# Kernel tuning notes

Hardware: AMD Instinct MI355X
Metric: run time of the kernel (lower is better)

## Reference

```python
import jax, jax.numpy as jnp
import numpy as np

H, D, C, GROUPS = 8, 80, 640, 32
EPS = 1e-5


def group_norm(x, gamma, beta):
    b, h, w, c = x.shape
    xr = x.reshape(b, h, w, GROUPS, c // GROUPS)
    mean = xr.mean(axis=(1, 2, 4), keepdims=True)
    var = xr.var(axis=(1, 2, 4), keepdims=True)
    xn = ((xr - mean) * jax.lax.rsqrt(var + EPS)).reshape(b, h, w, c)
    return xn * gamma + beta


def layer_norm(x, gamma, beta):
    mean = x.mean(axis=-1, keepdims=True)
    var = x.var(axis=-1, keepdims=True)
    return (x - mean) * jax.lax.rsqrt(var + EPS) * gamma + beta


def cross_attention(x, ctx, wq, wk, wv, wo, bo):
    b, sq, _ = x.shape
    sk = ctx.shape[1]
    q = (x @ wq).reshape(b, sq, H, D)
    k = (ctx @ wk).reshape(b, sk, H, D)
    v = (ctx @ wv).reshape(b, sk, H, D)
    score = jnp.einsum('bqhd,bkhd->bhqk', q, k) * (D ** -0.5)
    w = jax.nn.softmax(score, axis=-1)
    attn = jnp.einsum('bhqk,bkhd->bqhd', w, v).reshape(b, sq, H * D)
    return attn @ wo + bo


def geglu(x, w, bias):
    y = x @ w + bias
    xx, gate = y[..., :4 * C], y[..., 4 * C:]
    tanh_res = jnp.tanh(gate * 0.7978845608 * (1.0 + 0.044715 * gate * gate))
    return xx * 0.5 * gate * (1.0 + tanh_res)


def setup_inputs() -> dict:
    key = jax.random.key(0)
    ks = jax.random.split(key, 32)
    s = 0.02
    inp = {
        'inputs': jax.random.normal(ks[0], (8, 32, 32, C), jnp.float32),
        'context': jax.random.normal(ks[1], (8, 77, 768), jnp.float32),
        'gn_gamma': jnp.ones((C,), jnp.float32),
        'gn_beta': jnp.zeros((C,), jnp.float32),
        'w_proj1': jax.random.normal(ks[2], (C, C), jnp.float32) * s,
        'b_proj1': jnp.zeros((C,), jnp.float32),
        'ln1_g': jnp.ones((C,), jnp.float32), 'ln1_b': jnp.zeros((C,), jnp.float32),
        'wq1': jax.random.normal(ks[3], (C, C), jnp.float32) * s,
        'wk1': jax.random.normal(ks[4], (C, C), jnp.float32) * s,
        'wv1': jax.random.normal(ks[5], (C, C), jnp.float32) * s,
        'wo1': jax.random.normal(ks[6], (C, C), jnp.float32) * s,
        'bo1': jnp.zeros((C,), jnp.float32),
        'ln2_g': jnp.ones((C,), jnp.float32), 'ln2_b': jnp.zeros((C,), jnp.float32),
        'wq2': jax.random.normal(ks[7], (C, C), jnp.float32) * s,
        'wk2': jax.random.normal(ks[8], (768, C), jnp.float32) * s,
        'wv2': jax.random.normal(ks[9], (768, C), jnp.float32) * s,
        'wo2': jax.random.normal(ks[10], (C, C), jnp.float32) * s,
        'bo2': jnp.zeros((C,), jnp.float32),
        'ln3_g': jnp.ones((C,), jnp.float32), 'ln3_b': jnp.zeros((C,), jnp.float32),
        'w_geglu': jax.random.normal(ks[11], (C, 8 * C), jnp.float32) * s,
        'b_geglu': jnp.zeros((8 * C,), jnp.float32),
        'w_ffout': jax.random.normal(ks[12], (4 * C, C), jnp.float32) * s,
        'b_ffout': jnp.zeros((C,), jnp.float32),
        'w_proj2': jax.random.normal(ks[13], (C, C), jnp.float32) * s,
        'b_proj2': jnp.zeros((C,), jnp.float32),
    }
    return inp


def reference(inputs, context, gn_gamma, gn_beta, w_proj1, b_proj1,
              ln1_g, ln1_b, wq1, wk1, wv1, wo1, bo1,
              ln2_g, ln2_b, wq2, wk2, wv2, wo2, bo2,
              ln3_g, ln3_b, w_geglu, b_geglu, w_ffout, b_ffout,
              w_proj2, b_proj2):
    b, h, w, c = inputs.shape
    x = group_norm(inputs, gn_gamma, gn_beta)
    x = x @ w_proj1 + b_proj1  # 1x1 conv == per-pixel dense
    x = x.reshape(b, h * w, c)
    # BasicTransformerBlock
    x = cross_attention(layer_norm(x, ln1_g, ln1_b), layer_norm(x, ln1_g, ln1_b), wq1, wk1, wv1, wo1, bo1) + x
    x = cross_attention(layer_norm(x, ln2_g, ln2_b), context, wq2, wk2, wv2, wo2, bo2) + x
    x = geglu(layer_norm(x, ln3_g, ln3_b), w_geglu, b_geglu) @ w_ffout + b_ffout + x
    x = x.reshape(b, h, w, c)
    return x @ w_proj2 + b_proj2 + inputs
```

## Files before the change

### kernel.cpp

```cpp
#include <hip/hip_runtime.h>
#include <hip/hip_bf16.h>


#define HD 8
#define DHD 80
#define CCH 640
#define SQ 1024

using short8  = __attribute__((ext_vector_type(8))) short;
using floatx4 = __attribute__((ext_vector_type(4))) float;

__device__ __forceinline__ float bf2f(ushort u) {
  union { unsigned int i; float f; } v; v.i = ((unsigned int)u) << 16; return v.f;
}
__device__ __forceinline__ ushort f2bf(float f) {
  union { float f; unsigned int i; } v; v.f = f;
  unsigned int r = v.i + 0x7FFFu + ((v.i >> 16) & 1u);
  return (ushort)(r >> 16);
}
__device__ __forceinline__ float gelu_gate(float g) {
  float z = 0.7978845608f * g * (1.0f + 0.044715f * g * g);
  return g / (1.0f + __expf(-2.0f * z));
}

typedef const __attribute__((address_space(1))) void* gas_ptr;
typedef __attribute__((address_space(3))) void* las_ptr;
__device__ __forceinline__ void gload_lds16(const void* g, void* l) {
  __builtin_amdgcn_global_load_lds((gas_ptr)g, (las_ptr)l, 16, 0, 0);
}

template<int BN>
__global__ __launch_bounds__(256) void gemm_bf16_kernel(
    const ushort* __restrict__ A, const ushort* __restrict__ BT,
    const float* __restrict__ bias, const float* __restrict__ res,
    float* __restrict__ outF, ushort* __restrict__ outB,
    int M, int N, int K, int nby, int q8, int r8)
{
  constexpr int NT  = BN / 32;
  constexpr int LPT = (BN == 128) ? 4 : 3;
  __shared__ ushort As[3][128][32];
  __shared__ ushort Bs[3][BN][32];
  const int tid  = threadIdx.x;
  const int lane = tid & 63;
  const int wave = tid >> 6;
  const int wm = (wave >> 1) * 64, wn = (wave & 1) * (BN / 2);

  const int orig = blockIdx.x;
  const int xcd = orig & 7, bix = orig >> 3;
  const int logical = (xcd < r8) ? xcd * (q8 + 1) + bix
                                 : r8 * (q8 + 1) + (xcd - r8) * q8 + bix;
  const int bm = (logical / nby) * 128;
  const int bn = (logical % nby) * BN;

  const int fr = lane & 15, fk = (lane >> 4) * 8;
  const bool full = (bm + 128 <= M);
  const int nt = K >> 5;

  floatx4 acc[4][NT];
  #pragma unroll
  for (int i = 0; i < 4; ++i)
    #pragma unroll
    for (int j = 0; j < NT; ++j) acc[i][j] = (floatx4){0.f, 0.f, 0.f, 0.f};

  const int lr = lane >> 2, lc = (lane & 3) * 8;
  const ushort* pA0 = A  + (size_t)(bm + wave * 16 + lr) * K + lc;
  const ushort* pA1 = pA0 + (size_t)64 * K;
  const ushort* pB0 = BT + (size_t)(bn + wave * 16 + lr) * K + lc;
  const ushort* pB1 = pB0 + (size_t)64 * K;
  const int r0 = tid >> 2, c0 = (tid & 3) * 8;

  if (full) {
    auto stageF = [&](int nb, int t) {
      const int kt = t * 32;
      gload_lds16(pA0 + kt, &As[nb][wave * 16][0]);
      gload_lds16(pA1 + kt, &As[nb][wave * 16 + 64][0]);
      gload_lds16(pB0 + kt, &Bs[nb][wave * 16][0]);
      if (BN == 128) gload_lds16(pB1 + kt, &Bs[nb][wave * 16 + 64][0]);
    };
    stageF(0, 0);
    if (nt > 1) stageF(1, 1);
    int cb = 0;
    for (int t = 0; t < nt; ++t) {
      if (t + 1 < nt) {
        asm volatile("s_waitcnt vmcnt(%0)" :: "i"(LPT) : "memory");
      } else {
        asm volatile("s_waitcnt vmcnt(0)" ::: "memory");
      }
      __builtin_amdgcn_s_barrier();
      if (t + 2 < nt) stageF((cb + 2 > 2) ? cb - 1 : cb + 2, t + 2);
      short8 af[4], bfr[NT];
      #pragma unroll
      for (int mi = 0; mi < 4; ++mi) af[mi]  = *(const short8*)(&As[cb][wm + mi * 16 + fr][fk]);
      #pragma unroll
      for (int ni = 0; ni < NT; ++ni) bfr[ni] = *(const short8*)(&Bs[cb][wn + ni * 16 + fr][fk]);
      #pragma unroll
      for (int mi = 0; mi < 4; ++mi)
        #pragma unroll
        for (int ni = 0; ni < NT; ++ni)
          acc[mi][ni] = __builtin_amdgcn_mfma_f32_16x16x32_bf16(af[mi], bfr[ni], acc[mi][ni], 0, 0, 0);
      cb = (cb == 2) ? 0 : cb + 1;
    }
  } else {
    auto stageT = [&](int nb, int t) {
      const int kt = t * 32;
      #pragma unroll
      for (int it = 0; it < 2; ++it) {
        int r = r0 + it * 64;
        int gm = bm + r;
        uint4 va = make_uint4(0u, 0u, 0u, 0u);
        if (gm < M) va = *(const uint4*)(A + (size_t)gm * K + kt + c0);
        *(uint4*)(&As[nb][r][c0]) = va;
        if (r < BN) {
          int gn = bn + r;
          uint4 vb = make_uint4(0u, 0u, 0u, 0u);
          if (gn < N) vb = *(const uint4*)(BT + (size_t)gn * K + kt + c0);
          *(uint4*)(&Bs[nb][r][c0]) = vb;
        }
      }
    };
    stageT(0, 0);
    __syncthreads();
    int cur = 0;
    for (int t = 0; t < nt; ++t) {
      if (t + 1 < nt) stageT(cur ^ 1, t + 1);
      short8 af[4], bfr[NT];
      #pragma unroll
      for (int mi = 0; mi < 4; ++mi) af[mi]  = *(const short8*)(&As[cur][wm + mi * 16 + fr][fk]);
      #pragma unroll
      for (int ni = 0; ni < NT; ++ni) bfr[ni] = *(const short8*)(&Bs[cur][wn + ni * 16 + fr][fk]);
      #pragma unroll
      for (int mi = 0; mi < 4; ++mi)
        #pragma unroll
        for (int ni = 0; ni < NT; ++ni)
          acc[mi][ni] = __builtin_amdgcn_mfma_f32_16x16x32_bf16(af[mi], bfr[ni], acc[mi][ni], 0, 0, 0);
      __syncthreads();
      cur ^= 1;
    }
  }

  const int fq = (lane >> 4) * 4;
  #pragma unroll
  for (int mi = 0; mi < 4; ++mi)
    #pragma unroll
    for (int rr = 0; rr < 4; ++rr) {
      int gm = bm + wm + mi * 16 + fq + rr;
      if (gm >= M) continue;
      #pragma unroll
      for (int ni = 0; ni < NT; ++ni) {
        int col = bn + wn + ni * 16 + fr;
        float v = acc[mi][ni][rr];
        if (bias) v += bias[col];
        if (res) v += res[(size_t)gm * N + col];
        size_t o = (size_t)gm * N + col;
        if (outF) outF[o] = v;
        if (outB) outB[o] = f2bf(v);
      }
    }
}

__global__ __launch_bounds__(256) void gemm_geglu_kernel(
    const ushort* __restrict__ A, const ushort* __restrict__ BTx,
    const ushort* __restrict__ BTg, const float* __restrict__ bx,
    const float* __restrict__ bg, ushort* __restrict__ outB,
    int M, int N, int K, int nby, int q8, int r8)
{
  __shared__ ushort As[3][128][32];
  __shared__ ushort Bsx[3][64][32];
  __shared__ ushort Bsg[3][64][32];
  const int tid  = threadIdx.x;
  const int lane = tid & 63;
  const int wave = tid >> 6;
  const int wm = (wave >> 1) * 64, wn = (wave & 1) * 32;

  const int orig = blockIdx.x;
  const int xcd = orig & 7, bix = orig >> 3;
  const int logical = (xcd < r8) ? xcd * (q8 + 1) + bix
                                 : r8 * (q8 + 1) + (xcd - r8) * q8 + bix;
  const int bm = (logical / nby) * 128;
  const int bn = (logical % nby) * 64;

  const int fr = lane & 15, fk = (lane >> 4) * 8;
  const int nt = K >> 5;

  floatx4 accx[4][2], accg[4][2];
  #pragma unroll
  for (int i = 0; i < 4; ++i)
    #pragma unroll
    for (int j = 0; j < 2; ++j) {
      accx[i][j] = (floatx4){0.f, 0.f, 0.f, 0.f};
      accg[i][j] = (floatx4){0.f, 0.f, 0.f, 0.f};
    }

  const int lr = lane >> 2, lc = (lane & 3) * 8;
  const ushort* pA0 = A   + (size_t)(bm + wave * 16 + lr) * K + lc;
  const ushort* pA1 = pA0 + (size_t)64 * K;
  const ushort* pBx = BTx + (size_t)(bn + wave * 16 + lr) * K + lc;
  const ushort* pBg = BTg + (size_t)(bn + wave * 16 + lr) * K + lc;

  auto stageF = [&](int nb, int t) {
    const int kt = t * 32;
    gload_lds16(pA0 + kt, &As[nb][wave * 16][0]);
    gload_lds16(pA1 + kt, &As[nb][wave * 16 + 64][0]);
    gload_lds16(pBx + kt, &Bsx[nb][wave * 16][0]);
    gload_lds16(pBg + kt, &Bsg[nb][wave * 16][0]);
  };
  stageF(0, 0);
  if (nt > 1) stageF(1, 1);
  int cb = 0;
  for (int t = 0; t < nt; ++t) {
    if (t + 1 < nt) {
      asm volatile("s_waitcnt vmcnt(4)" ::: "memory");
    } else {
      asm volatile("s_waitcnt vmcnt(0)" ::: "memory");
    }
    __builtin_amdgcn_s_barrier();
    if (t + 2 < nt) stageF((cb + 2 > 2) ? cb - 1 : cb + 2, t + 2);
    short8 af[4], bfx[2], bfg[2];
    #pragma unroll
    for (int mi = 0; mi < 4; ++mi) af[mi] = *(const short8*)(&As[cb][wm + mi * 16 + fr][fk]);
    #pragma unroll
    for (int ni = 0; ni < 2; ++ni) {
      bfx[ni] = *(const short8*)(&Bsx[cb][wn + ni * 16 + fr][fk]);
      bfg[ni] = *(const short8*)(&Bsg[cb][wn + ni * 16 + fr][fk]);
    }
    #pragma unroll
    for (int mi = 0; mi < 4; ++mi)
      #pragma unroll
      for (int ni = 0; ni < 2; ++ni) {
        accx[mi][ni] = __builtin_amdgcn_mfma_f32_16x16x32_bf16(af[mi], bfx[ni], accx[mi][ni], 0, 0, 0);
        accg[mi][ni] = __builtin_amdgcn_mfma_f32_16x16x32_bf16(af[mi], bfg[ni], accg[mi][ni], 0, 0, 0);
      }
    cb = (cb == 2) ? 0 : cb + 1;
  }

  const int fq = (lane >> 4) * 4;
  #pragma unroll
  for (int mi = 0; mi < 4; ++mi)
    #pragma unroll
    for (int rr = 0; rr < 4; ++rr) {
      int gm = bm + wm + mi * 16 + fq + rr;
      #pragma unroll
      for (int ni = 0; ni < 2; ++ni) {
        int col = bn + wn + ni * 16 + fr;
        float xx = accx[mi][ni][rr] + bx[col];
        float g  = accg[mi][ni][rr] + bg[col];
        outB[(size_t)gm * N + col] = f2bf(xx * gelu_gate(g));
      }
    }
}

#define KVB 64

__global__ __launch_bounds__(256) void attn_mfma_kernel(
    const ushort* __restrict__ Qp, int rsq,
    const ushort* __restrict__ Kp, const ushort* __restrict__ Vp, int rskv,
    ushort* __restrict__ O, int Sq, int Sk)
{
  __shared__ ushort Ks[KVB][104];
  __shared__ ushort Vt[80][88];
  __shared__ ushort Ps[4][16][88];
  const int tid  = threadIdx.x;
  const int lane = tid & 63;
  const int w    = tid >> 6;
  const int l15  = lane & 15;
  const int lg   = lane >> 4;
  const int nqt  = Sq >> 6;
  const int qt   = blockIdx.x % nqt;
  const int bh   = blockIdx.x / nqt;
  const int h    = bh & (HD - 1);
  const int b    = bh / HD;
  const int q0   = qt * 64 + w * 16;

  short8 qf[3];
  #pragma unroll
  for (int kc = 0; kc < 3; ++kc) {
    int d0 = kc * 32 + lg * 8;
    if (d0 < DHD)
      qf[kc] = *(const short8*)(Qp + (size_t)(b * Sq + q0 + l15) * rsq + h * DHD + d0);
    else
      qf[kc] = (short8){0, 0, 0, 0, 0, 0, 0, 0};
  }

  floatx4 oa[5];
  #pragma unroll
  for (int nt = 0; nt < 5; ++nt) oa[nt] = (floatx4){0.f, 0.f, 0.f, 0.f};
  float m[4], lsum[4];
  #pragma unroll
  for (int r = 0; r < 4; ++r) { m[r] = -1e30f; lsum[r] = 0.f; }

  for (int c = tid; c < 128; c += 256)
    *(uint4*)(&Ks[c >> 1][80 + (c & 1) * 8]) = make_uint4(0u, 0u, 0u, 0u);

  for (int kt = 0; kt < Sk; kt += KVB) {
    __syncthreads();
    for (int c = tid; c < 320; c += 256) {
      int row = c / 5, sub = c % 5;
      int kvg = kt + row;
      uint4 v = make_uint4(0u, 0u, 0u, 0u);
      if (kvg < Sk) v = *(const uint4*)(Kp + (size_t)(b * Sk + kvg) * rskv + h * DHD + sub * 8);
      *(uint4*)(&Ks[row][sub * 8]) = v;
    }
    for (int idx = tid; idx < 2560; idx += 256) {
      int d = idx % 80, kv2 = (idx / 80) * 2;
      int kvg = kt + kv2;
      uint pair = 0;
      if (kvg < Sk)     pair  = (uint)Vp[(size_t)(b * Sk + kvg) * rskv + h * DHD + d];
      if (kvg + 1 < Sk) pair |= ((uint)Vp[(size_t)(b * Sk + kvg + 1) * rskv + h * DHD + d]) << 16;
      *(uint*)(&Vt[d][kv2]) = pair;
    }
    __syncthreads();

    short8 kf[4][3];
    #pragma unroll
    for (int nt = 0; nt < 4; ++nt)
      #pragma unroll
      for (int kc = 0; kc < 3; ++kc)
        kf[nt][kc] = *(const short8*)(&Ks[nt * 16 + l15][kc * 32 + lg * 8]);
    floatx4 s[4];
    #pragma unroll
    for (int nt = 0; nt < 4; ++nt) s[nt] = (floatx4){0.f, 0.f, 0.f, 0.f};
    #pragma unroll
    for (int nt = 0; nt < 4; ++nt)
      #pragma unroll
      for (int kc = 0; kc < 3; ++kc)
        s[nt] = __builtin_amdgcn_mfma_f32_16x16x32_bf16(qf[kc], kf[nt][kc], s[nt], 0, 0, 0);

    const bool masked = (kt + KVB > Sk);
    #pragma unroll
    for (int r = 0; r < 4; ++r) {
      float sv[4];
      #pragma unroll
      for (int nt = 0; nt < 4; ++nt) {
        float t = s[nt][r];
        sv[nt] = (masked && (kt + nt * 16 + l15 >= Sk)) ? -1e30f : t;
      }
      float mx = fmaxf(fmaxf(sv[0], sv[1]), fmaxf(sv[2], sv[3]));
      mx = fmaxf(mx, __shfl_xor(mx, 1));
      mx = fmaxf(mx, __shfl_xor(mx, 2));
      mx = fmaxf(mx, __shfl_xor(mx, 4));
      mx = fmaxf(mx, __shfl_xor(mx, 8));
      float mn = fmaxf(m[r], mx);
      float al = __expf(m[r] - mn);
      m[r] = mn;
      float lt = 0.f;
      #pragma unroll
      for (int nt = 0; nt < 4; ++nt) {
        float p = __expf(sv[nt] - mn);
        lt += p;
        Ps[w][lg * 4 + r][nt * 16 + l15] = f2bf(p);
      }
      lt += __shfl_xor(lt, 1);
      lt += __shfl_xor(lt, 2);
      lt += __shfl_xor(lt, 4);
      lt += __shfl_xor(lt, 8);
      lsum[r] = lsum[r] * al + lt;
      #pragma unroll
      for (int nt = 0; nt < 5; ++nt) oa[nt][r] *= al;
    }

    short8 pf[2];
    #pragma unroll
    for (int kc2 = 0; kc2 < 2; ++kc2)
      pf[kc2] = *(const short8*)(&Ps[w][l15][kc2 * 32 + lg * 8]);
    #pragma unroll
    for (int kc2 = 0; kc2 < 2; ++kc2)
      #pragma unroll
      for (int nt = 0; nt < 5; ++nt) {
        short8 vf = *(const short8*)(&Vt[nt * 16 + l15][kc2 * 32 + lg * 8]);
        oa[nt] = __builtin_amdgcn_mfma_f32_16x16x32_bf16(pf[kc2], vf, oa[nt], 0, 0, 0);
      }
  }

  #pragma unroll
  for (int r = 0; r < 4; ++r) {
    float inv = 1.f / lsum[r];
    size_t row = (size_t)(b * Sq + q0 + lg * 4 + r) * CCH + h * DHD;
    #pragma unroll
    for (int nt = 0; nt < 5; ++nt)
      O[row + nt * 16 + l15] = f2bf(oa[nt][r] * inv);
  }
}

__global__ __launch_bounds__(256) void layernorm_kernel(
    const float* __restrict__ X, const float* __restrict__ g,
    const float* __restrict__ bt, ushort* __restrict__ out)
{
  int row  = blockIdx.x * 4 + (threadIdx.x >> 6);
  int lane = threadIdx.x & 63;
  const float* xr = X + (size_t)row * CCH;
  float v[10];
  float s = 0.f, ss = 0.f;
  #pragma unroll
  for (int i = 0; i < 10; ++i) {
    float x = xr[lane + i * 64];
    v[i] = x; s += x; ss += x * x;
  }
  #pragma unroll
  for (int msk = 1; msk < 64; msk <<= 1) { s += __shfl_xor(s, msk); ss += __shfl_xor(ss, msk); }
  float mean = s * (1.f / 640.f);
  float var  = ss * (1.f / 640.f) - mean * mean;
  float rs   = rsqrtf(var + 1e-5f);
  ushort* orow = out + (size_t)row * CCH;
  #pragma unroll
  for (int i = 0; i < 10; ++i) {
    int c = lane + i * 64;
    orow[c] = f2bf((v[i] - mean) * rs * g[c] + bt[c]);
  }
}

__global__ __launch_bounds__(256) void groupnorm_kernel(
    const float* __restrict__ X, const float* __restrict__ gamma,
    const float* __restrict__ beta, ushort* __restrict__ out)
{
  int b = blockIdx.x >> 5;
  int g = blockIdx.x & 31;
  int tid = threadIdx.x;
  const float* base = X + (size_t)b * SQ * CCH + g * 20;
  float s = 0.f, ss = 0.f;
  for (int p = tid; p < SQ; p += 256) {
    const float* rp = base + (size_t)p * CCH;
    #pragma unroll
    for (int c = 0; c < 20; ++c) { float x = rp[c]; s += x; ss += x * x; }
  }
  #pragma unroll
  for (int msk = 1; msk < 64; msk <<= 1) { s += __shfl_xor(s, msk); ss += __shfl_xor(ss, msk); }
  __shared__ float red[2][4];
  int lane = tid & 63, wv = tid >> 6;
  if (lane == 0) { red[0][wv] = s; red[1][wv] = ss; }
  __syncthreads();
  s  = red[0][0] + red[0][1] + red[0][2] + red[0][3];
  ss = red[1][0] + red[1][1] + red[1][2] + red[1][3];
  float mean = s * (1.f / 20480.f);
  float var  = ss * (1.f / 20480.f) - mean * mean;
  float rstd = rsqrtf(var + 1e-5f);
  ushort* ob = out + (size_t)b * SQ * CCH + g * 20;
  for (int p = tid; p < SQ; p += 256) {
    const float* rp = base + (size_t)p * CCH;
    ushort* op = ob + (size_t)p * CCH;
    #pragma unroll
    for (int c = 0; c < 20; ++c)
      op[c] = f2bf((rp[c] - mean) * rstd * gamma[g * 20 + c] + beta[g * 20 + c]);
  }
}

__global__ __launch_bounds__(256) void transpose_cast_kernel(
    const float* __restrict__ W, ushort* __restrict__ WT, int K, int ld,
    int coff, float scale)
{
  __shared__ float tile[32][33];
  const int tx = threadIdx.x, ty = threadIdx.y;
  const int k0 = blockIdx.x * 32, n0 = blockIdx.y * 32;
  #pragma unroll
  for (int i = 0; i < 4; ++i)
    tile[ty + i * 8][tx] = W[(size_t)(k0 + ty + i * 8) * ld + coff + n0 + tx];
  __syncthreads();
  #pragma unroll
  for (int i = 0; i < 4; ++i)
    WT[(size_t)(n0 + ty + i * 8) * K + k0 + tx] = f2bf(tile[tx][ty + i * 8] * scale);
}

__global__ void cast_kernel(const float* __restrict__ X, ushort* __restrict__ Y, int n)
{
  int i = (blockIdx.x * 256 + threadIdx.x) * 4;
  if (i < n) {
    float4 v = *(const float4*)(X + i);
    ushort4 o;
    o.x = f2bf(v.x); o.y = f2bf(v.y); o.z = f2bf(v.z); o.w = f2bf(v.w);
    *(ushort4*)(Y + i) = o;
  }
}

static inline void gemm(hipStream_t st, const ushort* A, const ushort* BT,
                        const float* bias, const float* res,
                        float* outF, ushort* outB, int M, int N, int K)
{
  int nbx = (M + 127) / 128;
  if (N % 128 == 0 && N > 640) {
    int nby = N / 128, nwg = nbx * nby;
    gemm_bf16_kernel<128><<<dim3(nwg), dim3(256), 0, st>>>(
        A, BT, bias, res, outF, outB, M, N, K, nby, nwg / 8, nwg % 8);
  } else {
    int nby = N / 64, nwg = nbx * nby;
    gemm_bf16_kernel<64><<<dim3(nwg), dim3(256), 0, st>>>(
        A, BT, bias, res, outF, outB, M, N, K, nby, nwg / 8, nwg % 8);
  }
}

extern "C" void kernel_launch(void* const* d_in, const int* in_sizes, int n_in,
                              void* d_out, int out_size, void* d_ws, size_t ws_size,
                              hipStream_t stream)
{
  const float* inputs  = (const float*)d_in[0];
  const float* context = (const float*)d_in[1];
  const float* gn_g    = (const float*)d_in[2];
  const float* gn_b    = (const float*)d_in[3];
  const float* w_proj1 = (const float*)d_in[4];
  const float* b_proj1 = (const float*)d_in[5];
  const float* ln1_g   = (const float*)d_in[6];
  const float* ln1_b   = (const float*)d_in[7];
  const float* wq1     = (const float*)d_in[8];
  const float* wk1     = (const float*)d_in[9];
  const float* wv1     = (const float*)d_in[10];
  const float* wo1     = (const float*)d_in[11];
  const float* bo1     = (const float*)d_in[12];
  const float* ln2_g   = (const float*)d_in[13];
  const float* ln2_b   = (const float*)d_in[14];
  const float* wq2     = (const float*)d_in[15];
  const float* wk2     = (const float*)d_in[16];
  const float* wv2     = (const float*)d_in[17];
  const float* wo2     = (const float*)d_in[18];
  const float* bo2     = (const float*)d_in[19];
  const float* ln3_g   = (const float*)d_in[20];
  const float* ln3_b   = (const float*)d_in[21];
  const float* w_geglu = (const float*)d_in[22];
  const float* b_geglu = (const float*)d_in[23];
  const float* w_ffout = (const float*)d_in[24];
  const float* b_ffout = (const float*)d_in[25];
  const float* w_proj2 = (const float*)d_in[26];
  const float* b_proj2 = (const float*)d_in[27];

  const float qscale = 0.11180339887498949f;

  char* p = (char*)d_ws;
  auto alloc = [&](size_t bytes) -> char* {
    char* r = p; p += (bytes + 255) & ~(size_t)255; return r;
  };
  ushort* wT_p1   = (ushort*)alloc(640 * 640 * 2);
  ushort* wT_qkv1 = (ushort*)alloc((size_t)1920 * 640 * 2);
  ushort* wT_o1   = (ushort*)alloc(640 * 640 * 2);
  ushort* wT_q2   = (ushort*)alloc(640 * 640 * 2);
  ushort* wT_kv2  = (ushort*)alloc((size_t)1280 * 768 * 2);
  ushort* wT_o2   = (ushort*)alloc(640 * 640 * 2);
  ushort* wT_gx   = (ushort*)alloc((size_t)2560 * 640 * 2);
  ushort* wT_gg   = (ushort*)alloc((size_t)2560 * 640 * 2);
  ushort* wT_ff   = (ushort*)alloc((size_t)640 * 2560 * 2);
  ushort* wT_p2   = (ushort*)alloc(640 * 640 * 2);
  ushort* ctxb    = (ushort*)alloc((size_t)616 * 768 * 2);
  float*  x       = (float*)alloc((size_t)8192 * 640 * 4);
  ushort* lnb     = (ushort*)alloc((size_t)8192 * 640 * 2);
  ushort* R       = (ushort*)alloc((size_t)8192 * 2560 * 2);
  ushort* kvb     = (ushort*)alloc((size_t)616 * 1280 * 2);
  ushort* qkvb = R;
  ushort* qbx  = R;
  ushort* hb   = R;
  ushort* ab   = lnb;

  auto T = [&](const float* W, ushort* WT, int K, int Nout, int ld, int coff, float sc) {
    dim3 g(K / 32, Nout / 32);
    transpose_cast_kernel<<<g, dim3(32, 8), 0, stream>>>(W, WT, K, ld, coff, sc);
  };
  T(w_proj1, wT_p1, 640, 640, 640, 0, 1.f);
  T(wq1, wT_qkv1,              640, 640, 640, 0, qscale);
  T(wk1, wT_qkv1 + 640 * 640,  640, 640, 640, 0, 1.f);
  T(wv1, wT_qkv1 + 1280 * 640, 640, 640, 640, 0, 1.f);
  T(wo1, wT_o1, 640, 640, 640, 0, 1.f);
  T(wq2, wT_q2, 640, 640, 640, 0, qscale);
  T(wk2, wT_kv2,             768, 640, 640, 0, 1.f);
  T(wv2, wT_kv2 + 640 * 768, 768, 640, 640, 0, 1.f);
  T(wo2, wT_o2, 640, 640, 640, 0, 1.f);
  T(w_geglu, wT_gx, 640, 2560, 5120, 0, 1.f);
  T(w_geglu, wT_gg, 640, 2560, 5120, 2560, 1.f);
  T(w_ffout, wT_ff, 2560, 640, 640, 0, 1.f);
  T(w_proj2, wT_p2, 640, 640, 640, 0, 1.f);
  cast_kernel<<<dim3((616 * 768 / 4 + 255) / 256), dim3(256), 0, stream>>>(context, ctxb, 616 * 768);

  groupnorm_kernel<<<dim3(256), dim3(256), 0, stream>>>(inputs, gn_g, gn_b, lnb);
  gemm(stream, lnb, wT_p1, b_proj1, nullptr, x, nullptr, 8192, 640, 640);

  layernorm_kernel<<<dim3(2048), dim3(256), 0, stream>>>(x, ln1_g, ln1_b, lnb);
  gemm(stream, lnb, wT_qkv1, nullptr, nullptr, nullptr, qkvb, 8192, 1920, 640);
  attn_mfma_kernel<<<dim3(1024), dim3(256), 0, stream>>>(qkvb, 1920, qkvb + 640, qkvb + 1280, 1920, ab, 1024, 1024);
  gemm(stream, ab, wT_o1, bo1, x, x, nullptr, 8192, 640, 640);

  layernorm_kernel<<<dim3(2048), dim3(256), 0, stream>>>(x, ln2_g, ln2_b, lnb);
  gemm(stream, lnb, wT_q2, nullptr, nullptr, nullptr, qbx, 8192, 640, 640);
  gemm(stream, ctxb, wT_kv2, nullptr, nullptr, nullptr, kvb, 616, 1280, 768);
  attn_mfma_kernel<<<dim3(1024), dim3(256), 0, stream>>>(qbx, 640, kvb, kvb + 640, 1280, ab, 1024, 77);
  gemm(stream, ab, wT_o2, bo2, x, x, nullptr, 8192, 640, 640);

  layernorm_kernel<<<dim3(2048), dim3(256), 0, stream>>>(x, ln3_g, ln3_b, lnb);
  {
    int nby = 2560 / 64, nwg = 64 * nby;
    gemm_geglu_kernel<<<dim3(nwg), dim3(256), 0, stream>>>(
        lnb, wT_gx, wT_gg, b_geglu, b_geglu + 2560, hb, 8192, 2560, 640,
        nby, nwg / 8, nwg % 8);
  }
  gemm(stream, hb, wT_ff, b_ffout, x, x, nullptr, 8192, 640, 2560);

  cast_kernel<<<dim3((8192 * 640 / 4 + 255) / 256), dim3(256), 0, stream>>>(x, lnb, 8192 * 640);
  gemm(stream, lnb, wT_p2, b_proj2, inputs, (float*)d_out, nullptr, 8192, 640, 640);
}
```

Baseline: 591.3 us.

## Transpose QK^T MFMA so each lane owns a query row for softmax

Swaps the MFMA operands so the score tile comes out transposed: each lane holds four key scores for a single query row. The online-softmax max and sum then reduce mostly inside the lane, with only two cross-lane shuffles each, instead of four shuffle rounds per row for four rows. Probabilities are packed and written to LDS as uint2 rather than scalar shorts. Rescale factors and the final normalizers are redistributed to the output layout with __shfl. The V-transpose staging loop is also unrolled with incremental index updates to avoid div/mod.

```diff
diff --git a/kernel.cpp b/kernel.cpp
--- a/kernel.cpp
+++ b/kernel.cpp
@@ -284,9 +284,7 @@
   floatx4 oa[5];
   #pragma unroll
   for (int nt = 0; nt < 5; ++nt) oa[nt] = (floatx4){0.f, 0.f, 0.f, 0.f};
-  float m[4], lsum[4];
-  #pragma unroll
-  for (int r = 0; r < 4; ++r) { m[r] = -1e30f; lsum[r] = 0.f; }
+  float m = -1e30f, lsum = 0.f;
 
   for (int c = tid; c < 128; c += 256)
     *(uint4*)(&Ks[c >> 1][80 + (c & 1) * 8]) = make_uint4(0u, 0u, 0u, 0u);
@@ -300,13 +298,19 @@
       if (kvg < Sk) v = *(const uint4*)(Kp + (size_t)(b * Sk + kvg) * rskv + h * DHD + sub * 8);
       *(uint4*)(&Ks[row][sub * 8]) = v;
     }
-    for (int idx = tid; idx < 2560; idx += 256) {
-      int d = idx % 80, kv2 = (idx / 80) * 2;
-      int kvg = kt + kv2;
-      uint pair = 0;
-      if (kvg < Sk)     pair  = (uint)Vp[(size_t)(b * Sk + kvg) * rskv + h * DHD + d];
-      if (kvg + 1 < Sk) pair |= ((uint)Vp[(size_t)(b * Sk + kvg + 1) * rskv + h * DHD + d]) << 16;
-      *(uint*)(&Vt[d][kv2]) = pair;
+    {
+      int d = tid % 80;
+      int kv2 = (tid / 80) * 2;
+      const ushort* vpb = Vp + (size_t)(b * Sk + kt) * rskv + h * DHD;
+      #pragma unroll
+      for (int it = 0; it < 10; ++it) {
+        int kvg = kt + kv2;
+        uint pair = 0;
+        if (kvg < Sk)     pair  = (uint)vpb[(size_t)kv2 * rskv + d];
+        if (kvg + 1 < Sk) pair |= ((uint)vpb[(size_t)(kv2 + 1) * rskv + d]) << 16;
+        *(uint*)(&Vt[d][kv2]) = pair;
+        if (d >= 64) { d -= 64; kv2 += 8; } else { d += 16; kv2 += 6; }
+      }
     }
     __syncthreads();
 
@@ -323,40 +327,50 @@
     for (int nt = 0; nt < 4; ++nt)
       #pragma unroll
       for (int kc = 0; kc < 3; ++kc)
-        s[nt] = __builtin_amdgcn_mfma_f32_16x16x32_bf16(qf[kc], kf[nt][kc], s[nt], 0, 0, 0);
-
-    const bool masked = (kt + KVB > Sk);
-    #pragma unroll
-    for (int r = 0; r < 4; ++r) {
-      float sv[4];
-      #pragma unroll
-      for (int nt = 0; nt < 4; ++nt) {
-        float t = s[nt][r];
-        sv[nt] = (masked && (kt + nt * 16 + l15 >= Sk)) ? -1e30f : t;
-      }
-      float mx = fmaxf(fmaxf(sv[0], sv[1]), fmaxf(sv[2], sv[3]));
-      mx = fmaxf(mx, __shfl_xor(mx, 1));
-      mx = fmaxf(mx, __shfl_xor(mx, 2));
-      mx = fmaxf(mx, __shfl_xor(mx, 4));
-      mx = fmaxf(mx, __shfl_xor(mx, 8));
-      float mn = fmaxf(m[r], mx);
-      float al = __expf(m[r] - mn);
-      m[r] = mn;
-      float lt = 0.f;
-      #pragma unroll
-      for (int nt = 0; nt < 4; ++nt) {
-        float p = __expf(sv[nt] - mn);
-        lt += p;
-        Ps[w][lg * 4 + r][nt * 16 + l15] = f2bf(p);
-      }
-      lt += __shfl_xor(lt, 1);
-      lt += __shfl_xor(lt, 2);
-      lt += __shfl_xor(lt, 4);
-      lt += __shfl_xor(lt, 8);
-      lsum[r] = lsum[r] * al + lt;
-      #pragma unroll
-      for (int nt = 0; nt < 5; ++nt) oa[nt][r] *= al;
-    }
+        s[nt] = __builtin_amdgcn_mfma_f32_16x16x32_bf16(kf[nt][kc], qf[kc], s[nt], 0, 0, 0);
+
+    if (kt + KVB > Sk) {
+      #pragma unroll
+      for (int nt = 0; nt < 4; ++nt)
+        #pragma unroll
+        for (int r = 0; r < 4; ++r)
+          if (kt + nt * 16 + lg * 4 + r >= Sk) s[nt][r] = -1e30f;
+    }
+
+    float cm = s[0][0];
+    #pragma unroll
+    for (int nt = 0; nt < 4; ++nt)
+      #pragma unroll
+      for (int r = 0; r < 4; ++r) cm = fmaxf(cm, s[nt][r]);
+    cm = fmaxf(cm, __shfl_xor(cm, 16));
+    cm = fmaxf(cm, __shfl_xor(cm, 32));
+    float mn = fmaxf(m, cm);
+    float al = __expf(m - mn);
+    m = mn;
+    float lt = 0.f;
+    #pragma unroll
+    for (int nt = 0; nt < 4; ++nt) {
+      float p0 = __expf(s[nt][0] - mn);
+      float p1 = __expf(s[nt][1] - mn);
+      float p2 = __expf(s[nt][2] - mn);
+      float p3 = __expf(s[nt][3] - mn);
+      lt += (p0 + p1) + (p2 + p3);
+      uint lo = (uint)f2bf(p0) | ((uint)f2bf(p1) << 16);
+      uint hi = (uint)f2bf(p2) | ((uint)f2bf(p3) << 16);
+      *(uint2*)(&Ps[w][l15][nt * 16 + lg * 4]) = make_uint2(lo, hi);
+    }
+    lt += __shfl_xor(lt, 16);
+    lt += __shfl_xor(lt, 32);
+    lsum = lsum * al + lt;
+
+    float alr[4];
+    #pragma unroll
+    for (int r = 0; r < 4; ++r)
+      alr[r] = __shfl(al, (lane & 48) + lg * 4 + r);
+    #pragma unroll
+    for (int nt = 0; nt < 5; ++nt)
+      #pragma unroll
+      for (int r = 0; r < 4; ++r) oa[nt][r] *= alr[r];
 
     short8 pf[2];
     #pragma unroll
@@ -371,13 +385,17 @@
       }
   }
 
+  float inv = 1.f / lsum;
+  float invr[4];
+  #pragma unroll
+  for (int r = 0; r < 4; ++r)
+    invr[r] = __shfl(inv, (lane & 48) + lg * 4 + r);
   #pragma unroll
   for (int r = 0; r < 4; ++r) {
-    float inv = 1.f / lsum[r];
     size_t row = (size_t)(b * Sq + q0 + lg * 4 + r) * CCH + h * DHD;
     #pragma unroll
     for (int nt = 0; nt < 5; ++nt)
-      O[row + nt * 16 + l15] = f2bf(oa[nt][r] * inv);
+      O[row + nt * 16 + l15] = f2bf(oa[nt][r] * invr[r]);
   }
 }
 
```

Measured after the change: 649.2 us. +9.8%, slower.
